# Performance work log

Hardware: AMD Instinct MI355X
Metric: run time of the kernel (lower is better)

Reference implementation:

```python
import jax, jax.numpy as jnp
import numpy as np

IH, IW = 256, 704
FH, FW = 32, 88
D_MIN, D_MAX, D_RES = 1.0, 60.0, 0.5
D = int(np.ceil((D_MAX - D_MIN) / D_RES))  # 118 depth bins
C_IN, HID, C_OUT = 256, 64, 80
N_R, N_THETA = 128, 256
BN_EPS = 1e-5


def _edges():
    # non-uniform polar grid: angular bins uniform, radial bins grow with r
    ang = np.linspace(-np.pi / 2, np.pi / 2, N_THETA + 1).astype(np.float32)
    t = np.linspace(0.0, 1.0, N_R + 1)
    rad = (D_MIN + (t ** 1.5) * (D_MAX - D_MIN)).astype(np.float32)
    return jnp.asarray(ang), jnp.asarray(rad)


def _frustum():
    # [D, fH, fW, 3] of (u, v, depth) samples in image space
    ds = np.arange(D_MIN, D_MAX, D_RES, dtype=np.float32)
    xs = np.linspace(0, IW - 1, FW, dtype=np.float32)
    ys = np.linspace(0, IH - 1, FH, dtype=np.float32)
    d = np.broadcast_to(ds[:, None, None], (D, FH, FW))
    x = np.broadcast_to(xs[None, None, :], (D, FH, FW))
    y = np.broadcast_to(ys[None, :, None], (D, FH, FW))
    return jnp.asarray(np.stack([x, y, d], axis=-1))


def _bn(x, g, b, m, v):
    # inference-mode BatchNorm2d over channel axis 1; x: [BN, C, H, W]
    inv = g / jnp.sqrt(v + BN_EPS)
    return x * inv[None, :, None, None] + (b - m * inv)[None, :, None, None]


def setup_inputs() -> dict:
    key = jax.random.key(0)
    ks = jax.random.split(key, 8)
    B, N = 2, 1
    x = jax.random.normal(ks[0], (B, N, C_IN, FH, FW), dtype=jnp.float32)
    # camera->lidar axis permutation: x_l = z_c, y_l = -x_c, z_l = -y_c
    R = jnp.asarray([[0.0, 0.0, 1.0], [-1.0, 0.0, 0.0], [0.0, -1.0, 0.0]], dtype=jnp.float32)
    camera2lidar_rots = jnp.broadcast_to(R, (B, N, 3, 3))
    camera2lidar_trans = jnp.zeros((B, N, 3), dtype=jnp.float32)
    K = jnp.asarray([[380.0, 0.0, IW / 2.0], [0.0, 380.0, IH / 2.0], [0.0, 0.0, 1.0]], dtype=jnp.float32)
    intrins = jnp.broadcast_to(K, (B, N, 3, 3))
    s = 0.02
    params = dict(
        w1=jax.random.normal(ks[1], (HID, C_IN), dtype=jnp.float32) * s,
        b1=jnp.zeros((HID,), dtype=jnp.float32),
        g1=jnp.ones((HID,), dtype=jnp.float32),
        be1=jnp.zeros((HID,), dtype=jnp.float32),
        m1=jax.random.normal(ks[2], (HID,), dtype=jnp.float32) * s,
        v1=jnp.abs(jax.random.normal(ks[3], (HID,), dtype=jnp.float32)) + 0.5,
        w2=jax.random.normal(ks[4], (D + C_OUT, HID), dtype=jnp.float32) * s,
        b2=jnp.zeros((D + C_OUT,), dtype=jnp.float32),
        g2=jnp.ones((D + C_OUT,), dtype=jnp.float32),
        be2=jnp.zeros((D + C_OUT,), dtype=jnp.float32),
        m2=jax.random.normal(ks[5], (D + C_OUT,), dtype=jnp.float32) * s,
        v2=jnp.abs(jax.random.normal(ks[6], (D + C_OUT,), dtype=jnp.float32)) + 0.5,
    )
    return dict(x=x, camera2lidar_rots=camera2lidar_rots,
                camera2lidar_trans=camera2lidar_trans, intrins=intrins, **params)


def reference(x, camera2lidar_rots, camera2lidar_trans, intrins,
              w1, b1, g1, be1, m1, v1, w2, b2, g2, be2, m2, v2):
    B, N = x.shape[0], x.shape[1]
    # --- LIFT: DepthNet (two 1x1 convs + BN) -> depth dist x features outer product ---
    xf = x.reshape(B * N, C_IN, FH, FW)
    h = jnp.einsum('bchw,oc->bohw', xf, w1) + b1[None, :, None, None]
    h = jax.nn.relu(_bn(h, g1, be1, m1, v1))
    h = jnp.einsum('bchw,oc->bohw', h, w2) + b2[None, :, None, None]
    h = _bn(h, g2, be2, m2, v2)
    depth = jax.nn.softmax(h[:, :D], axis=1)            # [BN, D, fH, fW]
    feat = h[:, D:D + C_OUT]                            # [BN, C, fH, fW]
    lifted = depth[:, None, :, :, :] * feat[:, :, None, :, :]   # [BN, C, D, fH, fW]
    lifted = lifted.reshape(B, N, C_OUT, D, FH, FW).transpose(0, 1, 3, 4, 5, 2)  # [B,N,D,fH,fW,C]

    # --- geometry: unproject frustum to lidar frame ---
    fr = _frustum()                                      # [D, fH, fW, 3]
    u, v_, d = fr[..., 0], fr[..., 1], fr[..., 2]
    fx = intrins[..., 0, 0][:, :, None, None, None]
    fy = intrins[..., 1, 1][:, :, None, None, None]
    cx = intrins[..., 0, 2][:, :, None, None, None]
    cy = intrins[..., 1, 2][:, :, None, None, None]
    pc = jnp.stack([(u - cx) * d / fx, (v_ - cy) * d / fy,
                    jnp.broadcast_to(d, (B, N, D, FH, FW))], axis=-1)  # [B,N,D,fH,fW,3]
    pts = jnp.einsum('bnij,bndhwj->bndhwi', camera2lidar_rots, pc)
    pts = pts + camera2lidar_trans[:, :, None, None, None, :]

    # --- SPLAT: scatter-sum into non-uniform polar BEV grid ---
    ang_e, rad_e = _edges()
    xl, yl = pts[..., 0], pts[..., 1]
    r = jnp.sqrt(xl * xl + yl * yl)
    th = jnp.arctan2(yl, xl)
    r_idx = jnp.searchsorted(rad_e, r, side='right') - 1   # non-uniform bins -> bucketize
    t_idx = jnp.searchsorted(ang_e, th, side='right') - 1
    valid = (r_idx >= 0) & (r_idx < N_R) & (t_idx >= 0) & (t_idx < N_THETA)
    b_idx = jnp.arange(B)[:, None, None, None, None]
    trash = B * N_R * N_THETA  # dummy segment for out-of-grid points
    seg = jnp.where(valid, (b_idx * N_R + r_idx) * N_THETA + t_idx, trash).reshape(-1)
    bev = jax.ops.segment_sum(lifted.reshape(-1, C_OUT), seg, num_segments=trash + 1)[:-1]
    bev = bev.reshape(B, N_R, N_THETA, C_OUT).transpose(0, 3, 1, 2)  # [B, C, n_r, n_theta]
    return bev
```

## Files before the change

kernel.cpp:

```cpp
#include <hip/hip_runtime.h>
#include <hip/hip_bf16.h>
#include <math.h>

#define FH 32
#define FW 88
#define DD 118
#define C_IN 256
#define HID 64
#define C_OUT 80
#define NPIX 5632
#define PIX_PER_B 2816
#define N_R 128
#define N_THETA 256
#define NCOL 176
#define NBIN 32768
#define ECAP 12
#define PSTRIDE 9440

#define FRONT_MLP  352
#define FRONT_BINS 82
#define FRONT_ZERO 320
#define FRONT_TOTAL (FRONT_MLP + FRONT_BINS + FRONT_ZERO)

typedef __attribute__((ext_vector_type(8))) short short8;
typedef __attribute__((ext_vector_type(4))) float f32x4;

__device__ inline float bf2f(unsigned short h) {
  return __uint_as_float((unsigned)h << 16);
}
__device__ inline unsigned short f2bf(float f) {
  unsigned u = __float_as_uint(f);
  unsigned r = (u + 0x7fffu + ((u >> 16) & 1u)) >> 16;
  return (unsigned short)r;
}
__device__ inline bool detect_bf16(const void* intr) {
  float f = __uint_as_float(*(const unsigned*)intr);
  return !(f > 300.0f && f < 500.0f);
}
__device__ inline float ldf(const void* p, int i, bool isb) {
  return isb ? bf2f(((const unsigned short*)p)[i]) : ((const float*)p)[i];
}

__device__ inline void load_geom(int tid, float* radEL, float* angEL, float* camsL,
                                 const void* rots, const void* trans, const void* intr,
                                 bool isb) {
  if (tid < 129) {
    double t = (double)tid * (1.0 / 128.0);
    radEL[tid] = (float)(1.0 + pow(t, 1.5) * 59.0);
  }
  for (int i = tid; i < 257; i += 256) {
    double step = M_PI / 256.0;
    double vv = (i == 256) ? (M_PI / 2.0) : ((double)i * step + (-M_PI / 2.0));
    angEL[i] = (float)vv;
  }
  if (tid < 18) camsL[tid] = ldf(rots, tid, isb);
  if (tid < 6)  camsL[20 + tid] = ldf(trans, tid, isb);
  if (tid >= 6 && tid < 24) camsL[28 + (tid - 6)] = ldf(intr, tid - 6, isb);
}

__device__ inline int computeBin(int w, int h, int d,
                                 const float* camsF, int b,
                                 const float* radE, const float* angE) {
  float fx = camsF[28 + b * 9 + 0], cx = camsF[28 + b * 9 + 2];
  float fy = camsF[28 + b * 9 + 4], cy = camsF[28 + b * 9 + 5];
  float R00 = camsF[b * 9 + 0], R01 = camsF[b * 9 + 1], R02 = camsF[b * 9 + 2];
  float R10 = camsF[b * 9 + 3], R11 = camsF[b * 9 + 4], R12 = camsF[b * 9 + 5];
  float Tx = camsF[20 + b * 3 + 0], Ty = camsF[20 + b * 3 + 1];
  float u  = (w == FW - 1) ? 703.0f : (float)((double)w * (703.0 / 87.0));
  float vv = (h == FH - 1) ? 255.0f : (float)((double)h * (255.0 / 31.0));
  float dd = 1.0f + 0.5f * (float)d;
  float px = __fdiv_rn(__fmul_rn(__fsub_rn(u, cx), dd), fx);
  float py = __fdiv_rn(__fmul_rn(__fsub_rn(vv, cy), dd), fy);
  float xl = __fadd_rn(__fadd_rn(__fadd_rn(__fmul_rn(R00, px), __fmul_rn(R01, py)),
                                 __fmul_rn(R02, dd)), Tx);
  float yl = __fadd_rn(__fadd_rn(__fadd_rn(__fmul_rn(R10, px), __fmul_rn(R11, py)),
                                 __fmul_rn(R12, dd)), Ty);
  float r = __fsqrt_rn(__fadd_rn(__fmul_rn(xl, xl), __fmul_rn(yl, yl)));
  float th = (float)atan2((double)yl, (double)xl);
  int lo = 0, hi = 129;
  while (lo < hi) { int mid = (lo + hi) >> 1; if (radE[mid] <= r) lo = mid + 1; else hi = mid; }
  int ri = lo - 1;
  lo = 0; hi = 257;
  while (lo < hi) { int mid = (lo + hi) >> 1; if (angE[mid] <= th) lo = mid + 1; else hi = mid; }
  int ti = lo - 1;
  bool valid = (ri >= 0) && (ri < N_R) && (ti >= 0) && (ti < N_THETA);
  return valid ? (ri * N_THETA + ti) : -1;
}

__global__ __launch_bounds__(256) void k_front(
    const void* __restrict__ xraw,
    const void* __restrict__ rots, const void* __restrict__ trans,
    const void* __restrict__ intr,
    const void* __restrict__ w1r, const void* __restrict__ b1r,
    const void* __restrict__ g1r, const void* __restrict__ be1r,
    const void* __restrict__ m1r, const void* __restrict__ v1r,
    const void* __restrict__ w2r, const void* __restrict__ b2r,
    const void* __restrict__ g2r, const void* __restrict__ be2r,
    const void* __restrict__ m2r, const void* __restrict__ v2r,
    int* __restrict__ cnt, unsigned* __restrict__ ent, int* __restrict__ flag,
    float* __restrict__ depthW, float* __restrict__ featW,
    float* __restrict__ bevAcc) {
  __shared__ __align__(16) float shbuf[3712];
  __shared__ __align__(16) float h1L[16 * 68];
  __shared__ float inv1L[64], b1fL[64], inv2L[198], b2fL[198];
  __shared__ float radEL[129], angEL[257], camsL[46];

  int tid = threadIdx.x;
  bool isb = detect_bf16(intr);

  if (blockIdx.x >= FRONT_MLP + FRONT_BINS) {
    int zb = blockIdx.x - (FRONT_MLP + FRONT_BINS);
    float4 z = make_float4(0.f, 0.f, 0.f, 0.f);
    float4* bz = (float4*)bevAcc;
    int n4 = (NBIN * 2 * C_OUT) / 4;
    for (int i = zb * 256 + tid; i < n4; i += FRONT_ZERO * 256) bz[i] = z;
    return;
  }

  if (blockIdx.x >= FRONT_MLP) {
    int t = (blockIdx.x - FRONT_MLP) * 256 + tid;
    load_geom(tid, radEL, angEL, camsL, rots, trans, intr, isb);
    __syncthreads();
    if (t < NCOL * DD) {
      int col = t / DD, d = t - col * DD;
      int b = col / FW, w = col - b * FW;
      float R01 = camsL[b * 9 + 1], R11 = camsL[b * 9 + 4];
      if (!(R01 == 0.0f && R11 == 0.0f)) atomicOr(flag, 1);
      int bin = computeBin(w, 0, d, camsL, b, radEL, angEL);
      if (bin >= 0) {
        int slot = atomicAdd(&cnt[b * NBIN + bin], 1);
        if (slot < ECAP) ent[(size_t)(b * NBIN + bin) * ECAP + slot] = ((unsigned)col << 8) | (unsigned)d;
        else atomicOr(flag, 1);
      }
    }
    return;
  }

  unsigned short* xsU = (unsigned short*)shbuf;
  float* h2s = shbuf;
  float* smaxL = shbuf + 3200;
  float* ssumL = shbuf + 3456;
  if (tid < 64) {
    float iv = ldf(g1r, tid, isb) / sqrtf(ldf(v1r, tid, isb) + 1e-5f);
    inv1L[tid] = iv;
    b1fL[tid] = ldf(b1r, tid, isb) * iv + (ldf(be1r, tid, isb) - ldf(m1r, tid, isb) * iv);
  }
  if (tid < 198) {
    float iv = ldf(g2r, tid, isb) / sqrtf(ldf(v2r, tid, isb) + 1e-5f);
    inv2L[tid] = iv;
    b2fL[tid] = ldf(b2r, tid, isb) * iv + (ldf(be2r, tid, isb) - ldf(m2r, tid, isb) * iv);
  }
  int pix0 = blockIdx.x * 16;
  int b = pix0 / PIX_PER_B;
  int ploc0 = pix0 - b * PIX_PER_B;
  size_t xbase = (size_t)b * C_IN * PIX_PER_B + ploc0;
  const unsigned short* xh = (const unsigned short*)xraw;
  const float* xf = (const float*)xraw;
  {
    int p = tid & 15, crow = tid >> 4;
    for (int it = 0; it < 16; it++) {
      int c = it * 16 + crow;
      size_t gi = xbase + (size_t)c * PIX_PER_B + p;
      xsU[p * 264 + c] = isb ? xh[gi] : f2bf(xf[gi]);
    }
  }
  int lane = tid & 63, wv = tid >> 6;
  int nloc = lane & 15, quad = lane >> 4;
  int orow = wv * 16 + nloc;
  short8 afr[8];
  const unsigned short* w1h = (const unsigned short*)w1r;
  const float* w1f32 = (const float*)w1r;
  if (isb) {
#pragma unroll
    for (int s = 0; s < 8; s++)
      afr[s] = *(const short8*)(w1h + orow * 256 + s * 32 + quad * 8);
  } else {
#pragma unroll
    for (int s = 0; s < 8; s++) {
      short8 a;
#pragma unroll
      for (int j = 0; j < 8; j++)
        a[j] = (short)f2bf(w1f32[orow * 256 + s * 32 + quad * 8 + j]);
      afr[s] = a;
    }
  }
  __syncthreads();
  f32x4 acc = {0.f, 0.f, 0.f, 0.f};
#pragma unroll
  for (int s = 0; s < 8; s++) {
    short8 bfr = *(const short8*)(xsU + nloc * 264 + s * 32 + quad * 8);
    acc = __builtin_amdgcn_mfma_f32_16x16x32_bf16(afr[s], bfr, acc, 0, 0, 0);
  }
#pragma unroll
  for (int r = 0; r < 4; r++) {
    int m = wv * 16 + quad * 4 + r;
    float hv = fmaxf(fmaf(acc[r], inv1L[m], b1fL[m]), 0.f);
    h1L[nloc * 68 + m] = hv;
  }
  __syncthreads();
  int p = tid & 15, g = tid >> 4;
  float h1v[64];
  const float4* hp = (const float4*)(h1L + p * 68);
#pragma unroll
  for (int k4 = 0; k4 < 16; k4++) {
    float4 hv = hp[k4];
    h1v[4 * k4 + 0] = hv.x; h1v[4 * k4 + 1] = hv.y;
    h1v[4 * k4 + 2] = hv.z; h1v[4 * k4 + 3] = hv.w;
  }
  for (int j = 0; j < 13; j++) {
    int o = g * 13 + j;
    if (o < 198) {
      float iv = inv2L[o];
      float accs = b2fL[o];
      if (isb) {
        const ushort4* wr = (const ushort4*)w2r;
#pragma unroll
        for (int k4 = 0; k4 < 16; k4++) {
          ushort4 uw = wr[o * 16 + k4];
          accs = fmaf(bf2f(uw.x) * iv, h1v[4 * k4 + 0], accs);
          accs = fmaf(bf2f(uw.y) * iv, h1v[4 * k4 + 1], accs);
          accs = fmaf(bf2f(uw.z) * iv, h1v[4 * k4 + 2], accs);
          accs = fmaf(bf2f(uw.w) * iv, h1v[4 * k4 + 3], accs);
        }
      } else {
        const float4* wr = (const float4*)w2r;
#pragma unroll
        for (int k4 = 0; k4 < 16; k4++) {
          float4 w = wr[o * 16 + k4];
          accs = fmaf(w.x * iv, h1v[4 * k4 + 0], accs);
          accs = fmaf(w.y * iv, h1v[4 * k4 + 1], accs);
          accs = fmaf(w.z * iv, h1v[4 * k4 + 2], accs);
          accs = fmaf(w.w * iv, h1v[4 * k4 + 3], accs);
        }
      }
      h2s[o * 16 + p] = accs;
    }
  }
  __syncthreads();
  int r0 = g * 8, r1 = min(118, r0 + 8);
  float lm = -INFINITY;
  for (int o = r0; o < r1; o++) lm = fmaxf(lm, h2s[o * 16 + p]);
  smaxL[g * 16 + p] = lm;
  __syncthreads();
  float m = smaxL[p];
#pragma unroll
  for (int gg = 1; gg < 16; gg++) m = fmaxf(m, smaxL[gg * 16 + p]);
  float ls = 0.f;
  for (int o = r0; o < r1; o++) ls += expf(h2s[o * 16 + p] - m);
  ssumL[g * 16 + p] = ls;
  __syncthreads();
  float tot = 0.f;
#pragma unroll
  for (int gg = 0; gg < 16; gg++) tot += ssumL[gg * 16 + p];
  int pix = pix0 + p;
  for (int o = r0; o < r1; o++)
    depthW[(size_t)pix * DD + o] = expf(h2s[o * 16 + p] - m) / tot;
  int f0 = g * 5;
  for (int f = f0; f < f0 + 5; f++)
    featW[(size_t)pix * C_OUT + f] = h2s[(118 + f) * 16 + p];
}

__global__ __launch_bounds__(256) void k_back(const float* __restrict__ depthW,
                                              const float* __restrict__ featW,
                                              const int* __restrict__ flag,
                                              const void* __restrict__ rots,
                                              const void* __restrict__ trans,
                                              const void* __restrict__ intr,
                                              float* __restrict__ P,
                                              float* __restrict__ bevAcc) {
  __shared__ float depthL[DD * 33];
  __shared__ __align__(16) float featL[FH * C_OUT];
  __shared__ float radEL[129], angEL[257], camsL[46];
  __shared__ int flagS;
  int tid = threadIdx.x;
  if (tid == 0) flagS = *flag;
  __syncthreads();

  if (blockIdx.x < NCOL) {
    if (flagS != 0) return;
    int col = blockIdx.x;
    int b = col / FW, w = col - b * FW;
    size_t colPix = (size_t)b * PIX_PER_B + w;
    for (int i = tid; i < FH * DD; i += 256) {
      int h = i / DD, d = i - h * DD;
      depthL[d * 33 + h] = depthW[(colPix + (size_t)h * FW) * DD + d];
    }
    for (int i = tid; i < FH * C_OUT; i += 256) {
      int h = i / C_OUT, c = i - h * C_OUT;
      featL[i] = featW[(colPix + (size_t)h * FW) * C_OUT + c];
    }
    __syncthreads();
    const float4* featL4 = (const float4*)featL;
    float4* P4 = (float4*)(P + (size_t)col * PSTRIDE);
    for (int t = tid; t < DD * 20; t += 256) {
      int d = t / 20, c4 = t - d * 20;
      float4 a = make_float4(0.f, 0.f, 0.f, 0.f);
#pragma unroll
      for (int h = 0; h < FH; h++) {
        float wd = depthL[d * 33 + h];
        float4 f = featL4[h * 20 + c4];
        a.x = fmaf(wd, f.x, a.x); a.y = fmaf(wd, f.y, a.y);
        a.z = fmaf(wd, f.z, a.z); a.w = fmaf(wd, f.w, a.w);
      }
      P4[d * 20 + c4] = a;
    }
    return;
  }

  if (flagS == 0) return;
  bool isb = detect_bf16(intr);
  int idx2 = blockIdx.x - NCOL;
  int col = idx2 >> 1, chalf = idx2 & 1;
  int b = col / FW, w = col - b * FW;
  load_geom(tid, radEL, angEL, camsL, rots, trans, intr, isb);
  size_t colPix = (size_t)b * PIX_PER_B + w;
  for (int i = tid; i < FH * DD; i += 256) {
    int h = i / DD, d = i - h * DD;
    depthL[d * 33 + h] = depthW[(colPix + (size_t)h * FW) * DD + d];
  }
  for (int i = tid; i < FH * C_OUT; i += 256) {
    int h = i / C_OUT, c = i - h * C_OUT;
    featL[i] = featW[(colPix + (size_t)h * FW) * C_OUT + c];
  }
  __syncthreads();
  const float4* featL4 = (const float4*)featL;
  for (int t = tid; t < DD * FH * 10; t += 256) {
    int d = t / 320, rem = t - d * 320;
    int h = rem / 10, c4 = chalf * 10 + (rem - (rem / 10) * 10);
    int bin = computeBin(w, h, d, camsL, b, radEL, angEL);
    if (bin < 0) continue;
    float wd = depthL[d * 33 + h];
    float4 f = featL4[h * 20 + c4];
    float* outb = bevAcc + (((size_t)(b * C_OUT + c4 * 4)) << 15) + bin;
    unsafeAtomicAdd(outb, wd * f.x);
    unsafeAtomicAdd(outb + (1u << 15), wd * f.y);
    unsafeAtomicAdd(outb + (2u << 15), wd * f.z);
    unsafeAtomicAdd(outb + (3u << 15), wd * f.w);
  }
}

__global__ __launch_bounds__(256) void k_out(const float* __restrict__ P,
                                             const int* __restrict__ cnt,
                                             const unsigned* __restrict__ ent,
                                             const int* __restrict__ flag,
                                             const float* __restrict__ bevAcc,
                                             void* __restrict__ out,
                                             const void* __restrict__ intrRaw) {
  bool isb = detect_bf16(intrRaw);
  int tid = threadIdx.x;
  if (*flag != 0) {
    int idx = blockIdx.x * 256 + tid;
    const float4* a4 = (const float4*)bevAcc;
    int n4 = (NBIN * 2 * C_OUT) / 4;
    if (isb) {
      ushort4* o4 = (ushort4*)out;
      for (int i = idx; i < n4; i += 1024 * 256) {
        float4 v = a4[i];
        ushort4 o; o.x = f2bf(v.x); o.y = f2bf(v.y); o.z = f2bf(v.z); o.w = f2bf(v.w);
        o4[i] = o;
      }
    } else {
      float4* o4 = (float4*)out;
      for (int i = idx; i < n4; i += 1024 * 256) o4[i] = a4[i];
    }
    return;
  }
  int b = blockIdx.x >> 9;
  int ri = (blockIdx.x >> 2) & 127;
  int q = blockIdx.x & 3;
  int ti = tid;
  int bin = ri * N_THETA + ti;
  int n = cnt[b * NBIN + bin];
  if (n > ECAP) n = ECAP;
  unsigned ee[ECAP];
  const unsigned* eb = ent + (size_t)(b * NBIN + bin) * ECAP;
  for (int i = 0; i < n; i++) ee[i] = eb[i];
  for (int i = 1; i < n; i++) {
    unsigned key = ee[i]; int j = i - 1;
    while (j >= 0 && ee[j] > key) { ee[j + 1] = ee[j]; j--; }
    ee[j + 1] = key;
  }
  int base[ECAP];
  for (int i = 0; i < n; i++)
    base[i] = (int)(((ee[i] >> 8) * PSTRIDE + (ee[i] & 255u) * C_OUT) >> 2);
  const float4* P4 = (const float4*)P;
  unsigned short* oh = (unsigned short*)out;
  float* of = (float*)out;
  size_t obase = (((size_t)(b * C_OUT)) << 15) + bin;
  for (int c4 = q * 5; c4 < q * 5 + 5; c4++) {
    float4 s = make_float4(0.f, 0.f, 0.f, 0.f);
    for (int i = 0; i < n; i++) {
      float4 v = P4[base[i] + c4];
      s.x += v.x; s.y += v.y; s.z += v.z; s.w += v.w;
    }
    size_t o0 = obase + ((size_t)(c4 * 4) << 15);
    if (isb) {
      oh[o0]              = f2bf(s.x);
      oh[o0 + (1u << 15)] = f2bf(s.y);
      oh[o0 + (2u << 15)] = f2bf(s.z);
      oh[o0 + (3u << 15)] = f2bf(s.w);
    } else {
      of[o0]              = s.x;
      of[o0 + (1u << 15)] = s.y;
      of[o0 + (2u << 15)] = s.z;
      of[o0 + (3u << 15)] = s.w;
    }
  }
}

extern "C" void kernel_launch(void* const* d_in, const int* in_sizes, int n_in,
                              void* d_out, int out_size, void* d_ws, size_t ws_size,
                              hipStream_t stream) {
  const void* x     = d_in[0];
  const void* rots  = d_in[1];
  const void* trans = d_in[2];
  const void* intr  = d_in[3];
  const void* w1  = d_in[4];
  const void* b1  = d_in[5];
  const void* g1  = d_in[6];
  const void* be1 = d_in[7];
  const void* m1  = d_in[8];
  const void* v1  = d_in[9];
  const void* w2  = d_in[10];
  const void* b2  = d_in[11];
  const void* g2  = d_in[12];
  const void* be2 = d_in[13];
  const void* m2  = d_in[14];
  const void* v2  = d_in[15];

  float* ws = (float*)d_ws;
  float*    P      = ws + 0;
  int*      cnt    = (int*)(ws + 1661440);
  int*      flag   = (int*)(ws + 1726976);
  unsigned* ent    = (unsigned*)(ws + 1727040);
  float*    depthW = ws + 2513472;
  float*    featW  = ws + 3178048;
  float*    bevAcc = ws + 3628608;

  (void)hipMemsetAsync(cnt, 0, (size_t)(65536 + 64) * sizeof(int), stream);
  k_front<<<FRONT_TOTAL, 256, 0, stream>>>(x, rots, trans, intr,
                                           w1, b1, g1, be1, m1, v1,
                                           w2, b2, g2, be2, m2, v2,
                                           cnt, ent, flag, depthW, featW, bevAcc);
  k_back<<<NCOL * 3, 256, 0, stream>>>(depthW, featW, flag, rots, trans, intr, P, bevAcc);
  k_out<<<1024, 256, 0, stream>>>(P, cnt, ent, flag, bevAcc, d_out, intr);
}
```

Baseline: 142.6 us.

## Fuse memset and three kernels into one cooperative persistent kernel with grid syncs

Adds a cooperative persistent kernel that runs the counter clear, MLP and bin-list build, per-column product, and output gather as phases separated by grid-wide syncs, replacing the memset plus three launches. It also drops the unconditional zeroing of the large BEV accumulator on the common path and only zeroes it when the fallback scatter path is taken. The existing kernels are kept behind a fallback and refactored into shared device functions. The grid is capped at 512 blocks, so phases with more work than that loop over virtual blocks, and the grid syncs add their own cost in exchange for removing launch gaps.

```diff
diff --git a/kernel.cpp b/kernel.cpp
--- a/kernel.cpp
+++ b/kernel.cpp
@@ -1,6 +1,9 @@
 #include <hip/hip_runtime.h>
 #include <hip/hip_bf16.h>
+#include <hip/hip_cooperative_groups.h>
 #include <math.h>
+
+namespace cg = cooperative_groups;
 
 #define FH 32
 #define FW 88
@@ -87,6 +90,355 @@
   return valid ? (ri * N_THETA + ti) : -1;
 }
 
+
+__device__ __forceinline__ void dev_mlp(
+    int pix0, int tid, float* shbuf, float* h1L,
+    float* inv1L, float* b1fL, float* inv2L, float* b2fL,
+    const void* __restrict__ xraw,
+    const void* __restrict__ w1r, const void* __restrict__ b1r,
+    const void* __restrict__ g1r, const void* __restrict__ be1r,
+    const void* __restrict__ m1r, const void* __restrict__ v1r,
+    const void* __restrict__ w2r, const void* __restrict__ b2r,
+    const void* __restrict__ g2r, const void* __restrict__ be2r,
+    const void* __restrict__ m2r, const void* __restrict__ v2r,
+    float* __restrict__ depthW, float* __restrict__ featW, bool isb) {
+  unsigned short* xsU = (unsigned short*)shbuf;
+  float* h2s = shbuf;
+  float* smaxL = shbuf + 3200;
+  float* ssumL = shbuf + 3456;
+  if (tid < 64) {
+    float iv = ldf(g1r, tid, isb) / sqrtf(ldf(v1r, tid, isb) + 1e-5f);
+    inv1L[tid] = iv;
+    b1fL[tid] = ldf(b1r, tid, isb) * iv + (ldf(be1r, tid, isb) - ldf(m1r, tid, isb) * iv);
+  }
+  if (tid < 198) {
+    float iv = ldf(g2r, tid, isb) / sqrtf(ldf(v2r, tid, isb) + 1e-5f);
+    inv2L[tid] = iv;
+    b2fL[tid] = ldf(b2r, tid, isb) * iv + (ldf(be2r, tid, isb) - ldf(m2r, tid, isb) * iv);
+  }
+  int b = pix0 / PIX_PER_B;
+  int ploc0 = pix0 - b * PIX_PER_B;
+  size_t xbase = (size_t)b * C_IN * PIX_PER_B + ploc0;
+  const unsigned short* xh = (const unsigned short*)xraw;
+  const float* xf = (const float*)xraw;
+  {
+    int p = tid & 15, crow = tid >> 4;
+    for (int it = 0; it < 16; it++) {
+      int c = it * 16 + crow;
+      size_t gi = xbase + (size_t)c * PIX_PER_B + p;
+      xsU[p * 264 + c] = isb ? xh[gi] : f2bf(xf[gi]);
+    }
+  }
+  int lane = tid & 63, wv = tid >> 6;
+  int nloc = lane & 15, quad = lane >> 4;
+  int orow = wv * 16 + nloc;
+  short8 afr[8];
+  const unsigned short* w1h = (const unsigned short*)w1r;
+  const float* w1f32 = (const float*)w1r;
+  if (isb) {
+#pragma unroll
+    for (int s = 0; s < 8; s++)
+      afr[s] = *(const short8*)(w1h + orow * 256 + s * 32 + quad * 8);
+  } else {
+#pragma unroll
+    for (int s = 0; s < 8; s++) {
+      short8 a;
+#pragma unroll
+      for (int j = 0; j < 8; j++)
+        a[j] = (short)f2bf(w1f32[orow * 256 + s * 32 + quad * 8 + j]);
+      afr[s] = a;
+    }
+  }
+  __syncthreads();
+  f32x4 acc = {0.f, 0.f, 0.f, 0.f};
+#pragma unroll
+  for (int s = 0; s < 8; s++) {
+    short8 bfr = *(const short8*)(xsU + nloc * 264 + s * 32 + quad * 8);
+    acc = __builtin_amdgcn_mfma_f32_16x16x32_bf16(afr[s], bfr, acc, 0, 0, 0);
+  }
+#pragma unroll
+  for (int r = 0; r < 4; r++) {
+    int mm = wv * 16 + quad * 4 + r;
+    float hv = fmaxf(fmaf(acc[r], inv1L[mm], b1fL[mm]), 0.f);
+    h1L[nloc * 68 + mm] = hv;
+  }
+  __syncthreads();
+  int p = tid & 15, g = tid >> 4;
+  float h1v[64];
+  const float4* hp = (const float4*)(h1L + p * 68);
+#pragma unroll
+  for (int k4 = 0; k4 < 16; k4++) {
+    float4 hv = hp[k4];
+    h1v[4 * k4 + 0] = hv.x; h1v[4 * k4 + 1] = hv.y;
+    h1v[4 * k4 + 2] = hv.z; h1v[4 * k4 + 3] = hv.w;
+  }
+  for (int j = 0; j < 13; j++) {
+    int o = g * 13 + j;
+    if (o < 198) {
+      float iv = inv2L[o];
+      float accs = b2fL[o];
+      if (isb) {
+        const ushort4* wr = (const ushort4*)w2r;
+#pragma unroll
+        for (int k4 = 0; k4 < 16; k4++) {
+          ushort4 uw = wr[o * 16 + k4];
+          accs = fmaf(bf2f(uw.x) * iv, h1v[4 * k4 + 0], accs);
+          accs = fmaf(bf2f(uw.y) * iv, h1v[4 * k4 + 1], accs);
+          accs = fmaf(bf2f(uw.z) * iv, h1v[4 * k4 + 2], accs);
+          accs = fmaf(bf2f(uw.w) * iv, h1v[4 * k4 + 3], accs);
+        }
+      } else {
+        const float4* wr = (const float4*)w2r;
+#pragma unroll
+        for (int k4 = 0; k4 < 16; k4++) {
+          float4 w = wr[o * 16 + k4];
+          accs = fmaf(w.x * iv, h1v[4 * k4 + 0], accs);
+          accs = fmaf(w.y * iv, h1v[4 * k4 + 1], accs);
+          accs = fmaf(w.z * iv, h1v[4 * k4 + 2], accs);
+          accs = fmaf(w.w * iv, h1v[4 * k4 + 3], accs);
+        }
+      }
+      h2s[o * 16 + p] = accs;
+    }
+  }
+  __syncthreads();
+  int r0 = g * 8, r1 = min(118, r0 + 8);
+  float lm = -INFINITY;
+  for (int o = r0; o < r1; o++) lm = fmaxf(lm, h2s[o * 16 + p]);
+  smaxL[g * 16 + p] = lm;
+  __syncthreads();
+  float m = smaxL[p];
+#pragma unroll
+  for (int gg = 1; gg < 16; gg++) m = fmaxf(m, smaxL[gg * 16 + p]);
+  float ls = 0.f;
+  for (int o = r0; o < r1; o++) ls += expf(h2s[o * 16 + p] - m);
+  ssumL[g * 16 + p] = ls;
+  __syncthreads();
+  float tot = 0.f;
+#pragma unroll
+  for (int gg = 0; gg < 16; gg++) tot += ssumL[gg * 16 + p];
+  int pix = pix0 + p;
+  for (int o = r0; o < r1; o++)
+    depthW[(size_t)pix * DD + o] = expf(h2s[o * 16 + p] - m) / tot;
+  int f0 = g * 5;
+  for (int f = f0; f < f0 + 5; f++)
+    featW[(size_t)pix * C_OUT + f] = h2s[(118 + f) * 16 + p];
+}
+
+__device__ __forceinline__ void dev_bins(
+    int blk_rel, int tid, float* radEL, float* angEL, float* camsL,
+    const void* rots, const void* trans, const void* intr, bool isb,
+    int* __restrict__ cnt, unsigned* __restrict__ ent, int* __restrict__ flag) {
+  int t = blk_rel * 256 + tid;
+  load_geom(tid, radEL, angEL, camsL, rots, trans, intr, isb);
+  __syncthreads();
+  if (t < NCOL * DD) {
+    int col = t / DD, d = t - col * DD;
+    int b = col / FW, w = col - b * FW;
+    float R01 = camsL[b * 9 + 1], R11 = camsL[b * 9 + 4];
+    if (!(R01 == 0.0f && R11 == 0.0f)) atomicOr(flag, 1);
+    int bin = computeBin(w, 0, d, camsL, b, radEL, angEL);
+    if (bin >= 0) {
+      int slot = atomicAdd(&cnt[b * NBIN + bin], 1);
+      if (slot < ECAP) ent[(size_t)(b * NBIN + bin) * ECAP + slot] = ((unsigned)col << 8) | (unsigned)d;
+      else atomicOr(flag, 1);
+    }
+  }
+}
+
+__device__ __forceinline__ void dev_pcol(
+    int col, int tid, float* depthL, float* featL,
+    const float* __restrict__ depthW, const float* __restrict__ featW,
+    float* __restrict__ P) {
+  int b = col / FW, w = col - b * FW;
+  size_t colPix = (size_t)b * PIX_PER_B + w;
+  for (int i = tid; i < FH * DD; i += 256) {
+    int h = i / DD, d = i - h * DD;
+    depthL[d * 33 + h] = depthW[(colPix + (size_t)h * FW) * DD + d];
+  }
+  for (int i = tid; i < FH * C_OUT; i += 256) {
+    int h = i / C_OUT, c = i - h * C_OUT;
+    featL[i] = featW[(colPix + (size_t)h * FW) * C_OUT + c];
+  }
+  __syncthreads();
+  const float4* featL4 = (const float4*)featL;
+  float4* P4 = (float4*)(P + (size_t)col * PSTRIDE);
+  for (int t = tid; t < DD * 20; t += 256) {
+    int d = t / 20, c4 = t - d * 20;
+    float4 a = make_float4(0.f, 0.f, 0.f, 0.f);
+#pragma unroll
+    for (int h = 0; h < FH; h++) {
+      float wd = depthL[d * 33 + h];
+      float4 f = featL4[h * 20 + c4];
+      a.x = fmaf(wd, f.x, a.x); a.y = fmaf(wd, f.y, a.y);
+      a.z = fmaf(wd, f.z, a.z); a.w = fmaf(wd, f.w, a.w);
+    }
+    P4[d * 20 + c4] = a;
+  }
+}
+
+__device__ __forceinline__ void dev_scatter(
+    int idx2, int tid, float* depthL, float* featL,
+    float* radEL, float* angEL, float* camsL,
+    const void* rots, const void* trans, const void* intr, bool isb,
+    const float* __restrict__ depthW, const float* __restrict__ featW,
+    float* __restrict__ bevAcc) {
+  int col = idx2 >> 1, chalf = idx2 & 1;
+  int b = col / FW, w = col - b * FW;
+  load_geom(tid, radEL, angEL, camsL, rots, trans, intr, isb);
+  size_t colPix = (size_t)b * PIX_PER_B + w;
+  for (int i = tid; i < FH * DD; i += 256) {
+    int h = i / DD, d = i - h * DD;
+    depthL[d * 33 + h] = depthW[(colPix + (size_t)h * FW) * DD + d];
+  }
+  for (int i = tid; i < FH * C_OUT; i += 256) {
+    int h = i / C_OUT, c = i - h * C_OUT;
+    featL[i] = featW[(colPix + (size_t)h * FW) * C_OUT + c];
+  }
+  __syncthreads();
+  const float4* featL4 = (const float4*)featL;
+  for (int t = tid; t < DD * FH * 10; t += 256) {
+    int d = t / 320, rem = t - d * 320;
+    int h = rem / 10, c4 = chalf * 10 + (rem - (rem / 10) * 10);
+    int bin = computeBin(w, h, d, camsL, b, radEL, angEL);
+    if (bin < 0) continue;
+    float wd = depthL[d * 33 + h];
+    float4 f = featL4[h * 20 + c4];
+    float* outb = bevAcc + (((size_t)(b * C_OUT + c4 * 4)) << 15) + bin;
+    unsafeAtomicAdd(outb, wd * f.x);
+    unsafeAtomicAdd(outb + (1u << 15), wd * f.y);
+    unsafeAtomicAdd(outb + (2u << 15), wd * f.z);
+    unsafeAtomicAdd(outb + (3u << 15), wd * f.w);
+  }
+}
+
+__device__ __forceinline__ void dev_out_main(
+    int vt, int tid, const float* __restrict__ P,
+    const int* __restrict__ cnt, const unsigned* __restrict__ ent,
+    void* __restrict__ out, bool isb) {
+  int b = vt >> 9;
+  int ri = (vt >> 2) & 127;
+  int q = vt & 3;
+  int ti = tid;
+  int bin = ri * N_THETA + ti;
+  int n = cnt[b * NBIN + bin];
+  if (n > ECAP) n = ECAP;
+  unsigned ee[ECAP];
+  const unsigned* eb = ent + (size_t)(b * NBIN + bin) * ECAP;
+  for (int i = 0; i < n; i++) ee[i] = eb[i];
+  for (int i = 1; i < n; i++) {
+    unsigned key = ee[i]; int j = i - 1;
+    while (j >= 0 && ee[j] > key) { ee[j + 1] = ee[j]; j--; }
+    ee[j + 1] = key;
+  }
+  int base[ECAP];
+  for (int i = 0; i < n; i++)
+    base[i] = (int)(((ee[i] >> 8) * PSTRIDE + (ee[i] & 255u) * C_OUT) >> 2);
+  const float4* P4 = (const float4*)P;
+  unsigned short* oh = (unsigned short*)out;
+  float* of = (float*)out;
+  size_t obase = (((size_t)(b * C_OUT)) << 15) + bin;
+  for (int c4 = q * 5; c4 < q * 5 + 5; c4++) {
+    float4 s = make_float4(0.f, 0.f, 0.f, 0.f);
+    for (int i = 0; i < n; i++) {
+      float4 v = P4[base[i] + c4];
+      s.x += v.x; s.y += v.y; s.z += v.z; s.w += v.w;
+    }
+    size_t o0 = obase + ((size_t)(c4 * 4) << 15);
+    if (isb) {
+      oh[o0]              = f2bf(s.x);
+      oh[o0 + (1u << 15)] = f2bf(s.y);
+      oh[o0 + (2u << 15)] = f2bf(s.z);
+      oh[o0 + (3u << 15)] = f2bf(s.w);
+    } else {
+      of[o0]              = s.x;
+      of[o0 + (1u << 15)] = s.y;
+      of[o0 + (2u << 15)] = s.z;
+      of[o0 + (3u << 15)] = s.w;
+    }
+  }
+}
+
+__device__ __forceinline__ void dev_out_copy(
+    int gtid, int gstride, const float* __restrict__ bevAcc,
+    void* __restrict__ out, bool isb) {
+  const float4* a4 = (const float4*)bevAcc;
+  int n4 = (NBIN * 2 * C_OUT) / 4;
+  if (isb) {
+    ushort4* o4 = (ushort4*)out;
+    for (int i = gtid; i < n4; i += gstride) {
+      float4 v = a4[i];
+      ushort4 o; o.x = f2bf(v.x); o.y = f2bf(v.y); o.z = f2bf(v.z); o.w = f2bf(v.w);
+      o4[i] = o;
+    }
+  } else {
+    float4* o4 = (float4*)out;
+    for (int i = gtid; i < n4; i += gstride) o4[i] = a4[i];
+  }
+}
+
+__global__ __launch_bounds__(256) void k_fused(
+    const void* __restrict__ xraw,
+    const void* __restrict__ rots, const void* __restrict__ trans,
+    const void* __restrict__ intr,
+    const void* __restrict__ w1r, const void* __restrict__ b1r,
+    const void* __restrict__ g1r, const void* __restrict__ be1r,
+    const void* __restrict__ m1r, const void* __restrict__ v1r,
+    const void* __restrict__ w2r, const void* __restrict__ b2r,
+    const void* __restrict__ g2r, const void* __restrict__ be2r,
+    const void* __restrict__ m2r, const void* __restrict__ v2r,
+    int* __restrict__ cnt, unsigned* __restrict__ ent, int* __restrict__ flag,
+    float* __restrict__ depthW, float* __restrict__ featW,
+    float* __restrict__ bevAcc, float* __restrict__ P, void* __restrict__ out) {
+  __shared__ __align__(16) float SH[6464];
+  __shared__ float inv1L[64], b1fL[64], inv2L[198], b2fL[198];
+  __shared__ float radEL[129], angEL[257], camsL[46];
+  cg::grid_group grid = cg::this_grid();
+  int tid = threadIdx.x;
+  int bid = blockIdx.x, nb = gridDim.x;
+  bool isb = detect_bf16(intr);
+
+  for (int i = bid * 256 + tid; i < NBIN * 2 + 64; i += nb * 256) cnt[i] = 0;
+  grid.sync();
+
+  for (int vb = bid; vb < FRONT_MLP + FRONT_BINS; vb += nb) {
+    if (vb < FRONT_MLP) {
+      dev_mlp(vb * 16, tid, SH, SH + 3712, inv1L, b1fL, inv2L, b2fL,
+              xraw, w1r, b1r, g1r, be1r, m1r, v1r,
+              w2r, b2r, g2r, be2r, m2r, v2r, depthW, featW, isb);
+    } else {
+      dev_bins(vb - FRONT_MLP, tid, radEL, angEL, camsL,
+               rots, trans, intr, isb, cnt, ent, flag);
+    }
+    __syncthreads();
+  }
+  grid.sync();
+
+  int fl = *(volatile int*)flag;
+  if (fl == 0) {
+    for (int col = bid; col < NCOL; col += nb) {
+      dev_pcol(col, tid, SH, SH + 3896, depthW, featW, P);
+      __syncthreads();
+    }
+    grid.sync();
+    for (int vt = bid; vt < 1024; vt += nb)
+      dev_out_main(vt, tid, P, cnt, ent, out, isb);
+  } else {
+    float4 z = make_float4(0.f, 0.f, 0.f, 0.f);
+    float4* bz = (float4*)bevAcc;
+    int n4 = (NBIN * 2 * C_OUT) / 4;
+    for (int i = bid * 256 + tid; i < n4; i += nb * 256) bz[i] = z;
+    grid.sync();
+    for (int vt = bid; vt < NCOL * 2; vt += nb) {
+      dev_scatter(vt, tid, SH, SH + 3896, radEL, angEL, camsL,
+                  rots, trans, intr, isb, depthW, featW, bevAcc);
+      __syncthreads();
+    }
+    grid.sync();
+    dev_out_copy(bid * 256 + tid, nb * 256, bevAcc, out, isb);
+  }
+}
+
 __global__ __launch_bounds__(256) void k_front(
     const void* __restrict__ xraw,
     const void* __restrict__ rots, const void* __restrict__ trans,
@@ -104,10 +456,8 @@
   __shared__ __align__(16) float h1L[16 * 68];
   __shared__ float inv1L[64], b1fL[64], inv2L[198], b2fL[198];
   __shared__ float radEL[129], angEL[257], camsL[46];
-
   int tid = threadIdx.x;
   bool isb = detect_bf16(intr);
-
   if (blockIdx.x >= FRONT_MLP + FRONT_BINS) {
     int zb = blockIdx.x - (FRONT_MLP + FRONT_BINS);
     float4 z = make_float4(0.f, 0.f, 0.f, 0.f);
@@ -116,148 +466,14 @@
     for (int i = zb * 256 + tid; i < n4; i += FRONT_ZERO * 256) bz[i] = z;
     return;
   }
-
   if (blockIdx.x >= FRONT_MLP) {
-    int t = (blockIdx.x - FRONT_MLP) * 256 + tid;
-    load_geom(tid, radEL, angEL, camsL, rots, trans, intr, isb);
-    __syncthreads();
-    if (t < NCOL * DD) {
-      int col = t / DD, d = t - col * DD;
-      int b = col / FW, w = col - b * FW;
-      float R01 = camsL[b * 9 + 1], R11 = camsL[b * 9 + 4];
-      if (!(R01 == 0.0f && R11 == 0.0f)) atomicOr(flag, 1);
-      int bin = computeBin(w, 0, d, camsL, b, radEL, angEL);
-      if (bin >= 0) {
-        int slot = atomicAdd(&cnt[b * NBIN + bin], 1);
-        if (slot < ECAP) ent[(size_t)(b * NBIN + bin) * ECAP + slot] = ((unsigned)col << 8) | (unsigned)d;
-        else atomicOr(flag, 1);
-      }
-    }
+    dev_bins(blockIdx.x - FRONT_MLP, tid, radEL, angEL, camsL,
+             rots, trans, intr, isb, cnt, ent, flag);
     return;
   }
-
-  unsigned short* xsU = (unsigned short*)shbuf;
-  float* h2s = shbuf;
-  float* smaxL = shbuf + 3200;
-  float* ssumL = shbuf + 3456;
-  if (tid < 64) {
-    float iv = ldf(g1r, tid, isb) / sqrtf(ldf(v1r, tid, isb) + 1e-5f);
-    inv1L[tid] = iv;
-    b1fL[tid] = ldf(b1r, tid, isb) * iv + (ldf(be1r, tid, isb) - ldf(m1r, tid, isb) * iv);
-  }
-  if (tid < 198) {
-    float iv = ldf(g2r, tid, isb) / sqrtf(ldf(v2r, tid, isb) + 1e-5f);
-    inv2L[tid] = iv;
-    b2fL[tid] = ldf(b2r, tid, isb) * iv + (ldf(be2r, tid, isb) - ldf(m2r, tid, isb) * iv);
-  }
-  int pix0 = blockIdx.x * 16;
-  int b = pix0 / PIX_PER_B;
-  int ploc0 = pix0 - b * PIX_PER_B;
-  size_t xbase = (size_t)b * C_IN * PIX_PER_B + ploc0;
-  const unsigned short* xh = (const unsigned short*)xraw;
-  const float* xf = (const float*)xraw;
-  {
-    int p = tid & 15, crow = tid >> 4;
-    for (int it = 0; it < 16; it++) {
-      int c = it * 16 + crow;
-      size_t gi = xbase + (size_t)c * PIX_PER_B + p;
-      xsU[p * 264 + c] = isb ? xh[gi] : f2bf(xf[gi]);
-    }
-  }
-  int lane = tid & 63, wv = tid >> 6;
-  int nloc = lane & 15, quad = lane >> 4;
-  int orow = wv * 16 + nloc;
-  short8 afr[8];
-  const unsigned short* w1h = (const unsigned short*)w1r;
-  const float* w1f32 = (const float*)w1r;
-  if (isb) {
-#pragma unroll
-    for (int s = 0; s < 8; s++)
-      afr[s] = *(const short8*)(w1h + orow * 256 + s * 32 + quad * 8);
-  } else {
-#pragma unroll
-    for (int s = 0; s < 8; s++) {
-      short8 a;
-#pragma unroll
-      for (int j = 0; j < 8; j++)
-        a[j] = (short)f2bf(w1f32[orow * 256 + s * 32 + quad * 8 + j]);
-      afr[s] = a;
-    }
-  }
-  __syncthreads();
-  f32x4 acc = {0.f, 0.f, 0.f, 0.f};
-#pragma unroll
-  for (int s = 0; s < 8; s++) {
-    short8 bfr = *(const short8*)(xsU + nloc * 264 + s * 32 + quad * 8);
-    acc = __builtin_amdgcn_mfma_f32_16x16x32_bf16(afr[s], bfr, acc, 0, 0, 0);
-  }
-#pragma unroll
-  for (int r = 0; r < 4; r++) {
-    int m = wv * 16 + quad * 4 + r;
-    float hv = fmaxf(fmaf(acc[r], inv1L[m], b1fL[m]), 0.f);
-    h1L[nloc * 68 + m] = hv;
-  }
-  __syncthreads();
-  int p = tid & 15, g = tid >> 4;
-  float h1v[64];
-  const float4* hp = (const float4*)(h1L + p * 68);
-#pragma unroll
-  for (int k4 = 0; k4 < 16; k4++) {
-    float4 hv = hp[k4];
-    h1v[4 * k4 + 0] = hv.x; h1v[4 * k4 + 1] = hv.y;
-    h1v[4 * k4 + 2] = hv.z; h1v[4 * k4 + 3] = hv.w;
-  }
-  for (int j = 0; j < 13; j++) {
-    int o = g * 13 + j;
-    if (o < 198) {
-      float iv = inv2L[o];
-      float accs = b2fL[o];
-      if (isb) {
-        const ushort4* wr = (const ushort4*)w2r;
-#pragma unroll
-        for (int k4 = 0; k4 < 16; k4++) {
-          ushort4 uw = wr[o * 16 + k4];
-          accs = fmaf(bf2f(uw.x) * iv, h1v[4 * k4 + 0], accs);
-          accs = fmaf(bf2f(uw.y) * iv, h1v[4 * k4 + 1], accs);
-          accs = fmaf(bf2f(uw.z) * iv, h1v[4 * k4 + 2], accs);
-          accs = fmaf(bf2f(uw.w) * iv, h1v[4 * k4 + 3], accs);
-        }
-      } else {
-        const float4* wr = (const float4*)w2r;
-#pragma unroll
-        for (int k4 = 0; k4 < 16; k4++) {
-          float4 w = wr[o * 16 + k4];
-          accs = fmaf(w.x * iv, h1v[4 * k4 + 0], accs);
-          accs = fmaf(w.y * iv, h1v[4 * k4 + 1], accs);
-          accs = fmaf(w.z * iv, h1v[4 * k4 + 2], accs);
-          accs = fmaf(w.w * iv, h1v[4 * k4 + 3], accs);
-        }
-      }
-      h2s[o * 16 + p] = accs;
-    }
-  }
-  __syncthreads();
-  int r0 = g * 8, r1 = min(118, r0 + 8);
-  float lm = -INFINITY;
-  for (int o = r0; o < r1; o++) lm = fmaxf(lm, h2s[o * 16 + p]);
-  smaxL[g * 16 + p] = lm;
-  __syncthreads();
-  float m = smaxL[p];
-#pragma unroll
-  for (int gg = 1; gg < 16; gg++) m = fmaxf(m, smaxL[gg * 16 + p]);
-  float ls = 0.f;
-  for (int o = r0; o < r1; o++) ls += expf(h2s[o * 16 + p] - m);
-  ssumL[g * 16 + p] = ls;
-  __syncthreads();
-  float tot = 0.f;
-#pragma unroll
-  for (int gg = 0; gg < 16; gg++) tot += ssumL[gg * 16 + p];
-  int pix = pix0 + p;
-  for (int o = r0; o < r1; o++)
-    depthW[(size_t)pix * DD + o] = expf(h2s[o * 16 + p] - m) / tot;
-  int f0 = g * 5;
-  for (int f = f0; f < f0 + 5; f++)
-    featW[(size_t)pix * C_OUT + f] = h2s[(118 + f) * 16 + p];
+  dev_mlp(blockIdx.x * 16, tid, shbuf, h1L, inv1L, b1fL, inv2L, b2fL,
+          xraw, w1r, b1r, g1r, be1r, m1r, v1r,
+          w2r, b2r, g2r, be2r, m2r, v2r, depthW, featW, isb);
 }
 
 __global__ __launch_bounds__(256) void k_back(const float* __restrict__ depthW,
@@ -275,68 +491,15 @@
   int tid = threadIdx.x;
   if (tid == 0) flagS = *flag;
   __syncthreads();
-
   if (blockIdx.x < NCOL) {
     if (flagS != 0) return;
-    int col = blockIdx.x;
-    int b = col / FW, w = col - b * FW;
-    size_t colPix = (size_t)b * PIX_PER_B + w;
-    for (int i = tid; i < FH * DD; i += 256) {
-      int h = i / DD, d = i - h * DD;
-      depthL[d * 33 + h] = depthW[(colPix + (size_t)h * FW) * DD + d];
-    }
-    for (int i = tid; i < FH * C_OUT; i += 256) {
-      int h = i / C_OUT, c = i - h * C_OUT;
-      featL[i] = featW[(colPix + (size_t)h * FW) * C_OUT + c];
-    }
-    __syncthreads();
-    const float4* featL4 = (const float4*)featL;
-    float4* P4 = (float4*)(P + (size_t)col * PSTRIDE);
-    for (int t = tid; t < DD * 20; t += 256) {
-      int d = t / 20, c4 = t - d * 20;
-      float4 a = make_float4(0.f, 0.f, 0.f, 0.f);
-#pragma unroll
-      for (int h = 0; h < FH; h++) {
-        float wd = depthL[d * 33 + h];
-        float4 f = featL4[h * 20 + c4];
-        a.x = fmaf(wd, f.x, a.x); a.y = fmaf(wd, f.y, a.y);
-        a.z = fmaf(wd, f.z, a.z); a.w = fmaf(wd, f.w, a.w);
-      }
-      P4[d * 20 + c4] = a;
-    }
+    dev_pcol(blockIdx.x, tid, depthL, featL, depthW, featW, P);
     return;
   }
-
   if (flagS == 0) return;
   bool isb = detect_bf16(intr);
-  int idx2 = blockIdx.x - NCOL;
-  int col = idx2 >> 1, chalf = idx2 & 1;
-  int b = col / FW, w = col - b * FW;
-  load_geom(tid, radEL, angEL, camsL, rots, trans, intr, isb);
-  size_t colPix = (size_t)b * PIX_PER_B + w;
-  for (int i = tid; i < FH * DD; i += 256) {
-    int h = i / DD, d = i - h * DD;
-    depthL[d * 33 + h] = depthW[(colPix + (size_t)h * FW) * DD + d];
-  }
-  for (int i = tid; i < FH * C_OUT; i += 256) {
-    int h = i / C_OUT, c = i - h * C_OUT;
-    featL[i] = featW[(colPix + (size_t)h * FW) * C_OUT + c];
-  }
-  __syncthreads();
-  const float4* featL4 = (const float4*)featL;
-  for (int t = tid; t < DD * FH * 10; t += 256) {
-    int d = t / 320, rem = t - d * 320;
-    int h = rem / 10, c4 = chalf * 10 + (rem - (rem / 10) * 10);
-    int bin = computeBin(w, h, d, camsL, b, radEL, angEL);
-    if (bin < 0) continue;
-    float wd = depthL[d * 33 + h];
-    float4 f = featL4[h * 20 + c4];
-    float* outb = bevAcc + (((size_t)(b * C_OUT + c4 * 4)) << 15) + bin;
-    unsafeAtomicAdd(outb, wd * f.x);
-    unsafeAtomicAdd(outb + (1u << 15), wd * f.y);
-    unsafeAtomicAdd(outb + (2u << 15), wd * f.z);
-    unsafeAtomicAdd(outb + (3u << 15), wd * f.w);
-  }
+  dev_scatter(blockIdx.x - NCOL, tid, depthL, featL, radEL, angEL, camsL,
+              rots, trans, intr, isb, depthW, featW, bevAcc);
 }
 
 __global__ __launch_bounds__(256) void k_out(const float* __restrict__ P,
@@ -349,63 +512,10 @@
   bool isb = detect_bf16(intrRaw);
   int tid = threadIdx.x;
   if (*flag != 0) {
-    int idx = blockIdx.x * 256 + tid;
-    const float4* a4 = (const float4*)bevAcc;
-    int n4 = (NBIN * 2 * C_OUT) / 4;
-    if (isb) {
-      ushort4* o4 = (ushort4*)out;
-      for (int i = idx; i < n4; i += 1024 * 256) {
-        float4 v = a4[i];
-        ushort4 o; o.x = f2bf(v.x); o.y = f2bf(v.y); o.z = f2bf(v.z); o.w = f2bf(v.w);
-        o4[i] = o;
-      }
-    } else {
-      float4* o4 = (float4*)out;
-      for (int i = idx; i < n4; i += 1024 * 256) o4[i] = a4[i];
-    }
+    dev_out_copy(blockIdx.x * 256 + tid, 1024 * 256, bevAcc, out, isb);
     return;
   }
-  int b = blockIdx.x >> 9;
-  int ri = (blockIdx.x >> 2) & 127;
-  int q = blockIdx.x & 3;
-  int ti = tid;
-  int bin = ri * N_THETA + ti;
-  int n = cnt[b * NBIN + bin];
-  if (n > ECAP) n = ECAP;
-  unsigned ee[ECAP];
-  const unsigned* eb = ent + (size_t)(b * NBIN + bin) * ECAP;
-  for (int i = 0; i < n; i++) ee[i] = eb[i];
-  for (int i = 1; i < n; i++) {
-    unsigned key = ee[i]; int j = i - 1;
-    while (j >= 0 && ee[j] > key) { ee[j + 1] = ee[j]; j--; }
-    ee[j + 1] = key;
-  }
-  int base[ECAP];
-  for (int i = 0; i < n; i++)
-    base[i] = (int)(((ee[i] >> 8) * PSTRIDE + (ee[i] & 255u) * C_OUT) >> 2);
-  const float4* P4 = (const float4*)P;
-  unsigned short* oh = (unsigned short*)out;
-  float* of = (float*)out;
-  size_t obase = (((size_t)(b * C_OUT)) << 15) + bin;
-  for (int c4 = q * 5; c4 < q * 5 + 5; c4++) {
-    float4 s = make_float4(0.f, 0.f, 0.f, 0.f);
-    for (int i = 0; i < n; i++) {
-      float4 v = P4[base[i] + c4];
-      s.x += v.x; s.y += v.y; s.z += v.z; s.w += v.w;
-    }
-    size_t o0 = obase + ((size_t)(c4 * 4) << 15);
-    if (isb) {
-      oh[o0]              = f2bf(s.x);
-      oh[o0 + (1u << 15)] = f2bf(s.y);
-      oh[o0 + (2u << 15)] = f2bf(s.z);
-      oh[o0 + (3u << 15)] = f2bf(s.w);
-    } else {
-      of[o0]              = s.x;
-      of[o0 + (1u << 15)] = s.y;
-      of[o0 + (2u << 15)] = s.z;
-      of[o0 + (3u << 15)] = s.w;
-    }
-  }
+  dev_out_main(blockIdx.x, tid, P, cnt, ent, out, isb);
 }
 
 extern "C" void kernel_launch(void* const* d_in, const int* in_sizes, int n_in,
@@ -437,6 +547,36 @@
   float*    featW  = ws + 3178048;
   float*    bevAcc = ws + 3628608;
 
+  static int gblk = -2;
+  if (gblk == -2) {
+    int dev = 0;
+    (void)hipGetDevice(&dev);
+    int coop = 0, numCU = 0, maxb = 0;
+    (void)hipDeviceGetAttribute(&coop, hipDeviceAttributeCooperativeLaunch, dev);
+    (void)hipDeviceGetAttribute(&numCU, hipDeviceAttributeMultiprocessorCount, dev);
+    hipError_t e = hipOccupancyMaxActiveBlocksPerMultiprocessor(&maxb, (const void*)k_fused, 256, 0);
+    if (coop && e == hipSuccess && numCU > 0 && maxb > 0) {
+      long g = (long)maxb * (long)numCU;
+      gblk = (int)(g > 512 ? 512 : g);
+    } else {
+      gblk = -1;
+    }
+  }
+
+  if (gblk > 0) {
+    void* ka[24] = { (void*)&x, (void*)&rots, (void*)&trans, (void*)&intr,
+                     (void*)&w1, (void*)&b1, (void*)&g1, (void*)&be1,
+                     (void*)&m1, (void*)&v1, (void*)&w2, (void*)&b2,
+                     (void*)&g2, (void*)&be2, (void*)&m2, (void*)&v2,
+                     (void*)&cnt, (void*)&ent, (void*)&flag,
+                     (void*)&depthW, (void*)&featW, (void*)&bevAcc,
+                     (void*)&P, (void*)&d_out };
+    hipError_t e = hipLaunchCooperativeKernel((const void*)k_fused, dim3(gblk), dim3(256),
+                                              ka, 0u, stream);
+    if (e == hipSuccess) return;
+    gblk = -1;
+  }
+
   (void)hipMemsetAsync(cnt, 0, (size_t)(65536 + 64) * sizeof(int), stream);
   k_front<<<FRONT_TOTAL, 256, 0, stream>>>(x, rots, trans, intr,
                                            w1, b1, g1, be1, m1, v1,
```

Measured after the change: 142.7 us. Within noise of the previous version (+0.1%).
